# Kernel optimization log

Hardware: AMD Instinct MI355X
Metric: run time of the kernel (lower is better)

Reference implementation:

```python
import jax, jax.numpy as jnp
import numpy as np

N = 4096
D = 256
THRESH = 0.04  # default threshold arg of MultiLayerGCN.forward


def setup_inputs() -> dict:
    key = jax.random.key(0)
    ks = jax.random.split(key, 6)
    A = jax.random.normal(ks[0], (N, N), dtype=jnp.float32)
    features = jax.random.normal(ks[1], (N, D), dtype=jnp.float32)
    s = 0.02
    W1 = jax.random.normal(ks[2], (D, D), dtype=jnp.float32) * s
    b1 = jax.random.normal(ks[3], (D,), dtype=jnp.float32) * s
    W2 = jax.random.normal(ks[4], (D, D), dtype=jnp.float32) * s
    b2 = jax.random.normal(ks[5], (D,), dtype=jnp.float32) * s
    return {"A": A, "features": features, "W1": W1, "b1": b1, "W2": W2, "b2": b2}


def _graph_conv(C, out_isqrt, in_isqrt, h, W, b):
    # DGL GraphConv, norm='both': scale src by out_deg^-1/2, aggregate over
    # edges u->v (rst[v] = sum_u C[u,v] * h[u]), scale dst by in_deg^-1/2.
    h = (h * out_isqrt[:, None]) @ W            # [N, out]
    agg = jnp.einsum('uv,ud->vd', C, h)          # C^T @ h, honoring edge direction
    return agg * in_isqrt[:, None] + b


def reference(A, features, W1, b1, W2, b2):
    dt = features.dtype
    mask = (A >= THRESH).astype(dt)
    # add_edges(nodes, nodes) adds self loops on top of surviving diagonal -> counts
    C = mask + jnp.eye(A.shape[0], dtype=dt)
    out_deg = jnp.maximum(C.sum(axis=1), 1.0)    # clamp(min=1) as in DGL
    in_deg = jnp.maximum(C.sum(axis=0), 1.0)
    out_isqrt = jax.lax.rsqrt(out_deg)
    in_isqrt = jax.lax.rsqrt(in_deg)
    h1 = jax.nn.relu(_graph_conv(C, out_isqrt, in_isqrt, features, W1, b1))
    h2 = jax.nn.relu(_graph_conv(C, out_isqrt, in_isqrt, h1, W2, b2))
    return (h1, h2)
```

## Files before the change

kernel.cpp:

```cpp
#include <hip/hip_runtime.h>
#include <stdint.h>

#define NN 4096
#define DD 256
#define TH 0.04f

typedef __attribute__((ext_vector_type(4))) float f32x4;
typedef __attribute__((ext_vector_type(16))) float f32x16;
typedef __attribute__((ext_vector_type(8))) short s16x8;

__device__ __forceinline__ unsigned short f2bf(float f) {
  union { float f; uint32_t u; } x; x.f = f;
  uint32_t u = x.u;
  return (unsigned short)((u + 0x7FFFu + ((u >> 16) & 1u)) >> 16);
}
__device__ __forceinline__ float bf2f(unsigned short h) {
  union { uint32_t u; float f; } x; x.u = ((uint32_t)h) << 16;
  return x.f;
}

__global__ __launch_bounds__(256) void k_deg(const float* __restrict__ A,
                                             unsigned short* __restrict__ bitsT,
                                             unsigned char* __restrict__ colpart,
                                             float* __restrict__ oi,
                                             const float* __restrict__ W1,
                                             const float* __restrict__ W2,
                                             unsigned short* __restrict__ WTbP,
                                             unsigned short* __restrict__ W2TbP) {
  __shared__ unsigned short lds16[256 * 8];
  const int t = threadIdx.x, b = blockIdx.x;
  const int u0 = b * 8;
  uint32_t cs[16];
#pragma unroll
  for (int k = 0; k < 16; ++k) cs[k] = 0;
#pragma unroll
  for (int rb = 0; rb < 2; ++rb) {
    f32x4 a[4][4];
#pragma unroll
    for (int r = 0; r < 4; ++r) {
      const f32x4* p = reinterpret_cast<const f32x4*>(A + (size_t)(u0 + rb * 4 + r) * NN + t * 16);
#pragma unroll
      for (int c = 0; c < 4; ++c) a[r][c] = p[c];
    }
#pragma unroll
    for (int r = 0; r < 4; ++r) {
      uint32_t m = 0;
#pragma unroll
      for (int c = 0; c < 4; ++c)
#pragma unroll
        for (int j = 0; j < 4; ++j) m |= (a[r][c][j] >= TH ? 1u : 0u) << (c * 4 + j);
      lds16[t * 8 + rb * 4 + r] = (unsigned short)m;
#pragma unroll
      for (int k = 0; k < 16; ++k) cs[k] += (m >> k) & 1u;
    }
  }
  uint4 pk;
  pk.x = cs[0]  | (cs[1]  << 8) | (cs[2]  << 16) | (cs[3]  << 24);
  pk.y = cs[4]  | (cs[5]  << 8) | (cs[6]  << 16) | (cs[7]  << 24);
  pk.z = cs[8]  | (cs[9]  << 8) | (cs[10] << 16) | (cs[11] << 24);
  pk.w = cs[12] | (cs[13] << 8) | (cs[14] << 16) | (cs[15] << 24);
  *reinterpret_cast<uint4*>(colpart + (size_t)b * 4096 + t * 16) = pk;
  __syncthreads();
  uint4 wv4 = *reinterpret_cast<const uint4*>(&lds16[t * 8]);
  *reinterpret_cast<uint4*>(bitsT + (size_t)t * 4096 + u0) = wv4;
  if (t < 64) {
    const int r = t >> 3, part = t & 7;
    uint32_t s = 0;
#pragma unroll
    for (int wv = part * 32; wv < part * 32 + 32; ++wv)
      s += (uint32_t)__popc((uint32_t)lds16[wv * 8 + r]);
    s += __shfl_down(s, 4, 8);
    s += __shfl_down(s, 2, 8);
    s += __shfl_down(s, 1, 8);
    if (part == 0) oi[u0 + r] = rsqrtf((float)(s + 1u));
  }
  if (b < 32) {
    const float* W = (b < 16) ? W1 : W2;
    unsigned short* Wo = (b < 16) ? WTbP : W2TbP;
    const int base = (b & 15) * 4096 + t * 16;
#pragma unroll
    for (int e = 0; e < 16; ++e) {
      const int idx = base + e;
      const int frag = idx >> 9, pos = idx & 511;
      const int lc = pos >> 3, j = pos & 7;
      const int dt = frag >> 3, ks = frag & 7;
      const int k = ks * 32 + (lc >> 4) * 8 + j;
      const int d = dt * 16 + (lc & 15);
      Wo[idx] = f2bf(W[k * 256 + d]);
    }
  }
}

__global__ __launch_bounds__(256) void k_hw(const float* __restrict__ H,
                                            const float* __restrict__ oi,
                                            const unsigned short* __restrict__ WTbP,
                                            unsigned short* __restrict__ hWb,
                                            unsigned short* __restrict__ hWbP,
                                            const unsigned char* __restrict__ colpart,
                                            float* __restrict__ ii,
                                            int doii) {
  __shared__ unsigned short hs[16 * 264];
  __shared__ unsigned short lt[16 * 260];
  const int t = threadIdx.x;
  const int u0 = blockIdx.x * 16;
  if (doii) {
    const int v0 = blockIdx.x * 16;
    const int vI = t >> 4, g = t & 15;
    uint32_t s = 0;
#pragma unroll 8
    for (int r = g * 32; r < g * 32 + 32; ++r)
      s += colpart[(size_t)r * 4096 + v0 + vI];
    s += __shfl_down(s, 8, 16);
    s += __shfl_down(s, 4, 16);
    s += __shfl_down(s, 2, 16);
    s += __shfl_down(s, 1, 16);
    if (g == 0) ii[v0 + vI] = rsqrtf((float)(s + 1u));
  }
#pragma unroll
  for (int rep = 0; rep < 4; ++rep) {
    const int flat = rep * 256 + t;
    const int row = flat >> 6, c4 = flat & 63;
    f32x4 v = *reinterpret_cast<const f32x4*>(H + (size_t)(u0 + row) * DD + c4 * 4);
    const float sc = oi[u0 + row];
    uint2 pw;
    pw.x = (uint32_t)f2bf(v[0] * sc) | ((uint32_t)f2bf(v[1] * sc) << 16);
    pw.y = (uint32_t)f2bf(v[2] * sc) | ((uint32_t)f2bf(v[3] * sc) << 16);
    *reinterpret_cast<uint2*>(&hs[row * 264 + c4 * 4]) = pw;
  }
  __syncthreads();

  const int lane = t & 63, w = t >> 6, l15 = lane & 15, l4 = lane >> 4;
  const f32x4 z = {0.f, 0.f, 0.f, 0.f};
  f32x4 acc[4];
#pragma unroll
  for (int jn = 0; jn < 4; ++jn) acc[jn] = z;

#pragma unroll
  for (int ks = 0; ks < 8; ++ks) {
    s16x8 af = *reinterpret_cast<const s16x8*>(&hs[l15 * 264 + ks * 32 + l4 * 8]);
#pragma unroll
    for (int jn = 0; jn < 4; ++jn) {
      const int dt = w * 4 + jn;
      s16x8 bf = *reinterpret_cast<const s16x8*>(WTbP + ((size_t)dt * 8 + ks) * 512 + lane * 8);
      acc[jn] = __builtin_amdgcn_mfma_f32_16x16x32_bf16(af, bf, acc[jn], 0, 0, 0);
    }
  }
#pragma unroll
  for (int jn = 0; jn < 4; ++jn) {
    const int d = w * 64 + jn * 16 + l15;
#pragma unroll
    for (int r = 0; r < 4; ++r) {
      const int ul = l4 * 4 + r;
      unsigned short hv = f2bf(acc[jn][r]);
      hWb[(size_t)(u0 + ul) * DD + d] = hv;
      lt[ul * 260 + d] = hv;
    }
  }
  __syncthreads();
  const int sg = u0 >> 4;
#pragma unroll
  for (int cc = 0; cc < 2; ++cc) {
    const int c = t * 2 + cc;
    const int dt = c >> 6, lc = c & 63;
    const int ub = (lc >> 5) * 8;
    const int d = dt * 32 + (lc & 31);
    uint4 val;
    val.x = (uint32_t)lt[(ub + 0) * 260 + d] | ((uint32_t)lt[(ub + 1) * 260 + d] << 16);
    val.y = (uint32_t)lt[(ub + 2) * 260 + d] | ((uint32_t)lt[(ub + 3) * 260 + d] << 16);
    val.z = (uint32_t)lt[(ub + 4) * 260 + d] | ((uint32_t)lt[(ub + 5) * 260 + d] << 16);
    val.w = (uint32_t)lt[(ub + 6) * 260 + d] | ((uint32_t)lt[(ub + 7) * 260 + d] << 16);
    *reinterpret_cast<uint4*>(hWbP + ((size_t)dt * 256 + sg) * 512 + lc * 8) = val;
  }
}

__global__ __launch_bounds__(512, 2) void k_spmm(const unsigned short* __restrict__ bitsT,
                                                 const unsigned short* __restrict__ hWbP,
                                                 const unsigned short* __restrict__ hWb,
                                                 const float* __restrict__ ii,
                                                 const float* __restrict__ bias,
                                                 float* __restrict__ dst) {
  __shared__ float lds[4 * 64 * 68];
  const int t = threadIdx.x, bb = blockIdx.x;
  const int lane = t & 63, w = t >> 6;
  const int mi = w & 1, kc = w >> 1;
  const int xcd = bb & 7, jj = bb >> 3;
  const int vt = xcd * 8 + (jj >> 2), dq = jj & 3;
  const int V0 = vt * 64, D0 = dq * 64;
  const int l31 = lane & 31, l5 = lane >> 5;
  const uint32_t sh = lane & 15;
  const int wvl = vt * 4 + mi * 2 + ((lane >> 4) & 1);
  const unsigned short* Ab = bitsT + (size_t)wvl * 4096 + l5 * 8 + kc * 1024;
  const unsigned short* Bp0 = hWbP + ((size_t)(dq * 2 + 0) * 256 + kc * 64) * 512 + lane * 8;
  const unsigned short* Bp1 = hWbP + ((size_t)(dq * 2 + 1) * 256 + kc * 64) * 512 + lane * 8;

  f32x16 acc0, acc1;
#pragma unroll
  for (int q = 0; q < 16; ++q) { acc0[q] = 0.f; acc1[q] = 0.f; }

  uint4 h0 = *reinterpret_cast<const uint4*>(Ab);
  s16x8 p00 = *reinterpret_cast<const s16x8*>(Bp0);
  s16x8 p10 = *reinterpret_cast<const s16x8*>(Bp1);
  uint4 h1 = *reinterpret_cast<const uint4*>(Ab + 16);
  s16x8 p01 = *reinterpret_cast<const s16x8*>(Bp0 + 512);
  s16x8 p11 = *reinterpret_cast<const s16x8*>(Bp1 + 512);

#pragma unroll 1
  for (int it = 0; it < 32; ++it) {
    union { s16x8 v; uint32_t u[4]; } af0;
    af0.u[0] = ((h0.x >> sh) & 0x10001u) * 0x3F80u;
    af0.u[1] = ((h0.y >> sh) & 0x10001u) * 0x3F80u;
    af0.u[2] = ((h0.z >> sh) & 0x10001u) * 0x3F80u;
    af0.u[3] = ((h0.w >> sh) & 0x10001u) * 0x3F80u;
    acc0 = __builtin_amdgcn_mfma_f32_32x32x16_bf16(af0.v, p00, acc0, 0, 0, 0);
    acc1 = __builtin_amdgcn_mfma_f32_32x32x16_bf16(af0.v, p10, acc1, 0, 0, 0);
    const int s0 = (it * 2 + 2) & 63;
    h0 = *reinterpret_cast<const uint4*>(Ab + s0 * 16);
    p00 = *reinterpret_cast<const s16x8*>(Bp0 + s0 * 512);
    p10 = *reinterpret_cast<const s16x8*>(Bp1 + s0 * 512);
    union { s16x8 v; uint32_t u[4]; } af1;
    af1.u[0] = ((h1.x >> sh) & 0x10001u) * 0x3F80u;
    af1.u[1] = ((h1.y >> sh) & 0x10001u) * 0x3F80u;
    af1.u[2] = ((h1.z >> sh) & 0x10001u) * 0x3F80u;
    af1.u[3] = ((h1.w >> sh) & 0x10001u) * 0x3F80u;
    acc0 = __builtin_amdgcn_mfma_f32_32x32x16_bf16(af1.v, p01, acc0, 0, 0, 0);
    acc1 = __builtin_amdgcn_mfma_f32_32x32x16_bf16(af1.v, p11, acc1, 0, 0, 0);
    const int s1 = (it * 2 + 3) & 63;
    h1 = *reinterpret_cast<const uint4*>(Ab + s1 * 16);
    p01 = *reinterpret_cast<const s16x8*>(Bp0 + s1 * 512);
    p11 = *reinterpret_cast<const s16x8*>(Bp1 + s1 * 512);
  }

  float* buf = lds + (size_t)kc * (64 * 68);
#pragma unroll
  for (int reg = 0; reg < 16; ++reg) {
    const int row = (reg & 3) + 8 * (reg >> 2) + 4 * l5;
    buf[(mi * 32 + row) * 68 + l31] = acc0[reg];
    buf[(mi * 32 + row) * 68 + 32 + l31] = acc1[reg];
  }
  __syncthreads();

  const int vloc = t >> 3, d8 = (t & 7) * 8;
  const int v = V0 + vloc;
  const float* base = lds + vloc * 68 + d8;
  f32x4 s0v = *reinterpret_cast<const f32x4*>(base);
  f32x4 s1v = *reinterpret_cast<const f32x4*>(base + 4);
#pragma unroll
  for (int q = 1; q < 4; ++q) {
    s0v += *reinterpret_cast<const f32x4*>(base + q * (64 * 68));
    s1v += *reinterpret_cast<const f32x4*>(base + q * (64 * 68) + 4);
  }
  union { s16x8 v; unsigned short us[8]; } self;
  self.v = *reinterpret_cast<const s16x8*>(hWb + (size_t)v * DD + D0 + d8);
  const float iv = ii[v];
  const f32x4 bi0 = *reinterpret_cast<const f32x4*>(bias + D0 + d8);
  const f32x4 bi1 = *reinterpret_cast<const f32x4*>(bias + D0 + d8 + 4);
  f32x4 o0, o1;
#pragma unroll
  for (int e = 0; e < 4; ++e) {
    o0[e] = fmaxf((s0v[e] + bf2f(self.us[e])) * iv + bi0[e], 0.f);
    o1[e] = fmaxf((s1v[e] + bf2f(self.us[e + 4])) * iv + bi1[e], 0.f);
  }
  f32x4* po = reinterpret_cast<f32x4*>(dst + (size_t)v * DD + D0 + d8);
  po[0] = o0; po[1] = o1;
}

extern "C" void kernel_launch(void* const* d_in, const int* in_sizes, int n_in,
                              void* d_out, int out_size, void* d_ws, size_t ws_size,
                              hipStream_t stream) {
  const float* A    = (const float*)d_in[0];
  const float* feat = (const float*)d_in[1];
  const float* W1   = (const float*)d_in[2];
  const float* b1   = (const float*)d_in[3];
  const float* W2   = (const float*)d_in[4];
  const float* b2   = (const float*)d_in[5];
  float* out = (float*)d_out;
  char* ws = (char*)d_ws;

  unsigned short* bitsT   = (unsigned short*)ws;
  unsigned char*  colpart = (unsigned char*)(ws + (2u << 20));
  unsigned short* hWbP    = (unsigned short*)(ws + (4u << 20));
  unsigned short* hWb     = (unsigned short*)(ws + (6u << 20));
  unsigned short* WTbP    = (unsigned short*)(ws + (8u << 20));
  unsigned short* W2TbP   = (unsigned short*)(ws + (8u << 20) + (1u << 17));
  float*          oi      = (float*)(ws + (8u << 20) + (2u << 17));
  float*          ii      = oi + NN;

  k_deg<<<512, 256, 0, stream>>>(A, bitsT, colpart, oi, W1, W2, WTbP, W2TbP);

  k_hw<<<256, 256, 0, stream>>>(feat, oi, WTbP, hWb, hWbP, colpart, ii, 1);
  k_spmm<<<256, 512, 0, stream>>>(bitsT, hWbP, hWb, ii, b1, out);

  k_hw<<<256, 256, 0, stream>>>(out, oi, W2TbP, hWb, hWbP, colpart, ii, 0);
  k_spmm<<<256, 512, 0, stream>>>(bitsT, hWbP, hWb, ii, b2, out + (size_t)NN * DD);
}
```

Baseline: 75.00 us.

## Fuse first feature transform into scan kernel and move src-degree scaling into SpMM

Merges the threshold-scan kernel with the first H·W1 transform by giving extra blocks to the transform, which removes one launch and lets both stages overlap. The out-degree scaling is no longer applied to H before the GEMM. Instead a bf16 copy of out_isqrt is multiplied into the expanded adjacency bits inside the SpMM, and the self-loop term is scaled in the epilogue. In-degree computation moves from k_hw into the first SpMM. W is now converted and transposed through LDS per k-step inside each transform block rather than prepacked once, which adds redundant conversion work and extra syncs per block, and rounding out_isqrt to bf16 costs some accuracy.

```diff
diff --git a/kernel.cpp b/kernel.cpp
--- a/kernel.cpp
+++ b/kernel.cpp
@@ -8,26 +8,108 @@
 typedef __attribute__((ext_vector_type(4))) float f32x4;
 typedef __attribute__((ext_vector_type(16))) float f32x16;
 typedef __attribute__((ext_vector_type(8))) short s16x8;
-
-__device__ __forceinline__ unsigned short f2bf(float f) {
+typedef unsigned short us;
+
+__device__ __forceinline__ us f2bf(float f) {
   union { float f; uint32_t u; } x; x.f = f;
   uint32_t u = x.u;
-  return (unsigned short)((u + 0x7FFFu + ((u >> 16) & 1u)) >> 16);
-}
-__device__ __forceinline__ float bf2f(unsigned short h) {
+  return (us)((u + 0x7FFFu + ((u >> 16) & 1u)) >> 16);
+}
+__device__ __forceinline__ float bf2f(us h) {
   union { uint32_t u; float f; } x; x.u = ((uint32_t)h) << 16;
   return x.f;
 }
 
-__global__ __launch_bounds__(256) void k_deg(const float* __restrict__ A,
-                                             unsigned short* __restrict__ bitsT,
-                                             unsigned char* __restrict__ colpart,
-                                             float* __restrict__ oi,
-                                             const float* __restrict__ W1,
-                                             const float* __restrict__ W2,
-                                             unsigned short* __restrict__ WTbP,
-                                             unsigned short* __restrict__ W2TbP) {
-  __shared__ unsigned short lds16[256 * 8];
+__device__ __forceinline__ void hw_block(const float* __restrict__ H,
+                                         const float* __restrict__ W,
+                                         int u0,
+                                         us* __restrict__ hWb,
+                                         us* __restrict__ hWbP,
+                                         char* smem) {
+  us (*hs)[264] = reinterpret_cast<us(*)[264]>(smem);
+  us (*wt)[34]  = reinterpret_cast<us(*)[34]>(smem + 16 * 264 * 2);
+  us (*lt)[260] = reinterpret_cast<us(*)[260]>(smem + 16 * 264 * 2 + 256 * 34 * 2);
+  const int t = threadIdx.x;
+#pragma unroll
+  for (int rep = 0; rep < 4; ++rep) {
+    const int flat = rep * 256 + t;
+    const int row = flat >> 6, c4 = (flat & 63) * 4;
+    f32x4 v = *reinterpret_cast<const f32x4*>(H + (size_t)(u0 + row) * DD + c4);
+    uint2 pw;
+    pw.x = (uint32_t)f2bf(v[0]) | ((uint32_t)f2bf(v[1]) << 16);
+    pw.y = (uint32_t)f2bf(v[2]) | ((uint32_t)f2bf(v[3]) << 16);
+    *reinterpret_cast<uint2*>(&hs[row][c4]) = pw;
+  }
+  const int lane = t & 63, w = t >> 6, l15 = lane & 15, l4 = lane >> 4;
+  const f32x4 z = {0.f, 0.f, 0.f, 0.f};
+  f32x4 acc[4];
+#pragma unroll
+  for (int jn = 0; jn < 4; ++jn) acc[jn] = z;
+#pragma unroll 1
+  for (int ks = 0; ks < 8; ++ks) {
+    __syncthreads();
+#pragma unroll
+    for (int rr = 0; rr < 8; ++rr) {
+      const int flat = rr * 256 + t;
+      const int k = flat >> 6, d0 = (flat & 63) * 4;
+      f32x4 wv = *reinterpret_cast<const f32x4*>(W + (size_t)(ks * 32 + k) * DD + d0);
+      wt[d0 + 0][k] = f2bf(wv[0]);
+      wt[d0 + 1][k] = f2bf(wv[1]);
+      wt[d0 + 2][k] = f2bf(wv[2]);
+      wt[d0 + 3][k] = f2bf(wv[3]);
+    }
+    __syncthreads();
+    s16x8 af = *reinterpret_cast<const s16x8*>(&hs[l15][ks * 32 + l4 * 8]);
+#pragma unroll
+    for (int jn = 0; jn < 4; ++jn) {
+      const int dt = w * 4 + jn;
+      s16x8 bf = *reinterpret_cast<const s16x8*>(&wt[dt * 16 + l15][l4 * 8]);
+      acc[jn] = __builtin_amdgcn_mfma_f32_16x16x32_bf16(af, bf, acc[jn], 0, 0, 0);
+    }
+  }
+#pragma unroll
+  for (int jn = 0; jn < 4; ++jn) {
+    const int d = w * 64 + jn * 16 + l15;
+#pragma unroll
+    for (int r = 0; r < 4; ++r) {
+      const int ul = l4 * 4 + r;
+      us hv = f2bf(acc[jn][r]);
+      hWb[(size_t)(u0 + ul) * DD + d] = hv;
+      lt[ul][d] = hv;
+    }
+  }
+  __syncthreads();
+  const int sg = u0 >> 4;
+#pragma unroll
+  for (int cc = 0; cc < 2; ++cc) {
+    const int c = t * 2 + cc;
+    const int dt = c >> 6, lc = c & 63;
+    const int ub = (lc >> 5) * 8;
+    const int d = dt * 32 + (lc & 31);
+    uint4 val;
+    val.x = (uint32_t)lt[ub + 0][d] | ((uint32_t)lt[ub + 1][d] << 16);
+    val.y = (uint32_t)lt[ub + 2][d] | ((uint32_t)lt[ub + 3][d] << 16);
+    val.z = (uint32_t)lt[ub + 4][d] | ((uint32_t)lt[ub + 5][d] << 16);
+    val.w = (uint32_t)lt[ub + 6][d] | ((uint32_t)lt[ub + 7][d] << 16);
+    *reinterpret_cast<uint4*>(hWbP + ((size_t)dt * 256 + sg) * 512 + lc * 8) = val;
+  }
+}
+
+__global__ __launch_bounds__(256) void k_scanhw1(const float* __restrict__ A,
+                                                 const float* __restrict__ feat,
+                                                 const float* __restrict__ W1,
+                                                 us* __restrict__ bitsT,
+                                                 unsigned char* __restrict__ colpart,
+                                                 float* __restrict__ oif,
+                                                 us* __restrict__ oib,
+                                                 us* __restrict__ hWb,
+                                                 us* __restrict__ hWbP) {
+  __shared__ __align__(16) char smem[34176];
+  if (blockIdx.x >= 512) {
+    hw_block(feat, W1, (blockIdx.x - 512) * 16, hWb, hWbP, smem);
+    return;
+  }
+  us* lds16 = reinterpret_cast<us*>(smem);
   const int t = threadIdx.x, b = blockIdx.x;
   const int u0 = b * 8;
   uint32_t cs[16];
@@ -49,7 +131,7 @@
       for (int c = 0; c < 4; ++c)
 #pragma unroll
         for (int j = 0; j < 4; ++j) m |= (a[r][c][j] >= TH ? 1u : 0u) << (c * 4 + j);
-      lds16[t * 8 + rb * 4 + r] = (unsigned short)m;
+      lds16[t * 8 + rb * 4 + r] = (us)m;
 #pragma unroll
       for (int k = 0; k < 16; ++k) cs[k] += (m >> k) & 1u;
     }
@@ -72,170 +154,138 @@
     s += __shfl_down(s, 4, 8);
     s += __shfl_down(s, 2, 8);
     s += __shfl_down(s, 1, 8);
-    if (part == 0) oi[u0 + r] = rsqrtf((float)(s + 1u));
-  }
-  if (b < 32) {
-    const float* W = (b < 16) ? W1 : W2;
-    unsigned short* Wo = (b < 16) ? WTbP : W2TbP;
-    const int base = (b & 15) * 4096 + t * 16;
-#pragma unroll
-    for (int e = 0; e < 16; ++e) {
-      const int idx = base + e;
-      const int frag = idx >> 9, pos = idx & 511;
-      const int lc = pos >> 3, j = pos & 7;
-      const int dt = frag >> 3, ks = frag & 7;
-      const int k = ks * 32 + (lc >> 4) * 8 + j;
-      const int d = dt * 16 + (lc & 15);
-      Wo[idx] = f2bf(W[k * 256 + d]);
+    if (part == 0) {
+      float val = rsqrtf((float)(s + 1u));
+      oif[u0 + r] = val;
+      oib[u0 + r] = f2bf(val);
     }
   }
 }
 
 __global__ __launch_bounds__(256) void k_hw(const float* __restrict__ H,
-                                            const float* __restrict__ oi,
-                                            const unsigned short* __restrict__ WTbP,
-                                            unsigned short* __restrict__ hWb,
-                                            unsigned short* __restrict__ hWbP,
-                                            const unsigned char* __restrict__ colpart,
-                                            float* __restrict__ ii,
-                                            int doii) {
-  __shared__ unsigned short hs[16 * 264];
-  __shared__ unsigned short lt[16 * 260];
-  const int t = threadIdx.x;
-  const int u0 = blockIdx.x * 16;
-  if (doii) {
-    const int v0 = blockIdx.x * 16;
-    const int vI = t >> 4, g = t & 15;
-    uint32_t s = 0;
-#pragma unroll 8
-    for (int r = g * 32; r < g * 32 + 32; ++r)
-      s += colpart[(size_t)r * 4096 + v0 + vI];
-    s += __shfl_down(s, 8, 16);
-    s += __shfl_down(s, 4, 16);
-    s += __shfl_down(s, 2, 16);
-    s += __shfl_down(s, 1, 16);
-    if (g == 0) ii[v0 + vI] = rsqrtf((float)(s + 1u));
-  }
-#pragma unroll
-  for (int rep = 0; rep < 4; ++rep) {
-    const int flat = rep * 256 + t;
-    const int row = flat >> 6, c4 = flat & 63;
-    f32x4 v = *reinterpret_cast<const f32x4*>(H + (size_t)(u0 + row) * DD + c4 * 4);
-    const float sc = oi[u0 + row];
-    uint2 pw;
-    pw.x = (uint32_t)f2bf(v[0] * sc) | ((uint32_t)f2bf(v[1] * sc) << 16);
-    pw.y = (uint32_t)f2bf(v[2] * sc) | ((uint32_t)f2bf(v[3] * sc) << 16);
-    *reinterpret_cast<uint2*>(&hs[row * 264 + c4 * 4]) = pw;
-  }
-  __syncthreads();
-
-  const int lane = t & 63, w = t >> 6, l15 = lane & 15, l4 = lane >> 4;
-  const f32x4 z = {0.f, 0.f, 0.f, 0.f};
-  f32x4 acc[4];
-#pragma unroll
-  for (int jn = 0; jn < 4; ++jn) acc[jn] = z;
-
-#pragma unroll
-  for (int ks = 0; ks < 8; ++ks) {
-    s16x8 af = *reinterpret_cast<const s16x8*>(&hs[l15 * 264 + ks * 32 + l4 * 8]);
-#pragma unroll
-    for (int jn = 0; jn < 4; ++jn) {
-      const int dt = w * 4 + jn;
-      s16x8 bf = *reinterpret_cast<const s16x8*>(WTbP + ((size_t)dt * 8 + ks) * 512 + lane * 8);
-      acc[jn] = __builtin_amdgcn_mfma_f32_16x16x32_bf16(af, bf, acc[jn], 0, 0, 0);
-    }
-  }
-#pragma unroll
-  for (int jn = 0; jn < 4; ++jn) {
-    const int d = w * 64 + jn * 16 + l15;
-#pragma unroll
-    for (int r = 0; r < 4; ++r) {
-      const int ul = l4 * 4 + r;
-      unsigned short hv = f2bf(acc[jn][r]);
-      hWb[(size_t)(u0 + ul) * DD + d] = hv;
-      lt[ul * 260 + d] = hv;
-    }
-  }
-  __syncthreads();
-  const int sg = u0 >> 4;
-#pragma unroll
-  for (int cc = 0; cc < 2; ++cc) {
-    const int c = t * 2 + cc;
-    const int dt = c >> 6, lc = c & 63;
-    const int ub = (lc >> 5) * 8;
-    const int d = dt * 32 + (lc & 31);
-    uint4 val;
-    val.x = (uint32_t)lt[(ub + 0) * 260 + d] | ((uint32_t)lt[(ub + 1) * 260 + d] << 16);
-    val.y = (uint32_t)lt[(ub + 2) * 260 + d] | ((uint32_t)lt[(ub + 3) * 260 + d] << 16);
-    val.z = (uint32_t)lt[(ub + 4) * 260 + d] | ((uint32_t)lt[(ub + 5) * 260 + d] << 16);
-    val.w = (uint32_t)lt[(ub + 6) * 260 + d] | ((uint32_t)lt[(ub + 7) * 260 + d] << 16);
-    *reinterpret_cast<uint4*>(hWbP + ((size_t)dt * 256 + sg) * 512 + lc * 8) = val;
-  }
-}
-
-__global__ __launch_bounds__(512, 2) void k_spmm(const unsigned short* __restrict__ bitsT,
-                                                 const unsigned short* __restrict__ hWbP,
-                                                 const unsigned short* __restrict__ hWb,
-                                                 const float* __restrict__ ii,
+                                            const float* __restrict__ W,
+                                            us* __restrict__ hWb,
+                                            us* __restrict__ hWbP) {
+  __shared__ __align__(16) char smem[34176];
+  hw_block(H, W, blockIdx.x * 16, hWb, hWbP, smem);
+}
+
+__global__ __launch_bounds__(512, 2) void k_spmm(const us* __restrict__ bitsT,
+                                                 const us* __restrict__ hWbP,
+                                                 const us* __restrict__ hWb,
+                                                 const float* __restrict__ oif,
+                                                 const us* __restrict__ oib,
+                                                 const unsigned char* __restrict__ colpart,
+                                                 float* __restrict__ ii_g,
                                                  const float* __restrict__ bias,
-                                                 float* __restrict__ dst) {
+                                                 float* __restrict__ dst,
+                                                 int doii) {
   __shared__ float lds[4 * 64 * 68];
+  __shared__ float ii_s[64];
   const int t = threadIdx.x, bb = blockIdx.x;
   const int lane = t & 63, w = t >> 6;
-  const int mi = w & 1, kc = w >> 1;
+  const int kc = w >> 1, dn = w & 1;
   const int xcd = bb & 7, jj = bb >> 3;
   const int vt = xcd * 8 + (jj >> 2), dq = jj & 3;
   const int V0 = vt * 64, D0 = dq * 64;
+
+  if (doii) {
+    uint32_t* sc = reinterpret_cast<uint32_t*>(lds);
+    const int v4 = t & 15, c = t >> 4;
+    uint32_t s0 = 0, s1 = 0;
+#pragma unroll 4
+    for (int r = 0; r < 16; ++r) {
+      uint32_t x = *reinterpret_cast<const uint32_t*>(colpart + (size_t)(c * 16 + r) * 4096 + V0 + v4 * 4);
+      s0 += x & 0x00FF00FFu;
+      s1 += (x >> 8) & 0x00FF00FFu;
+    }
+    sc[(c * 16 + v4) * 2] = s0;
+    sc[(c * 16 + v4) * 2 + 1] = s1;
+    __syncthreads();
+    if (t < 64) {
+      const int v4b = t >> 2, sub = t & 3;
+      const int reg = sub & 1, hi = sub >> 1;
+      uint32_t s = 0;
+#pragma unroll
+      for (int cc = 0; cc < 32; ++cc)
+        s += (sc[(cc * 16 + v4b) * 2 + reg] >> (hi * 16)) & 0xFFFFu;
+      float val = rsqrtf((float)(s + 1u));
+      ii_s[t] = val;
+      ii_g[V0 + t] = val;
+    }
+    __syncthreads();
+  } else {
+    if (t < 64) ii_s[t] = ii_g[V0 + t];
+    __syncthreads();
+  }
+
   const int l31 = lane & 31, l5 = lane >> 5;
   const uint32_t sh = lane & 15;
-  const int wvl = vt * 4 + mi * 2 + ((lane >> 4) & 1);
-  const unsigned short* Ab = bitsT + (size_t)wvl * 4096 + l5 * 8 + kc * 1024;
-  const unsigned short* Bp0 = hWbP + ((size_t)(dq * 2 + 0) * 256 + kc * 64) * 512 + lane * 8;
-  const unsigned short* Bp1 = hWbP + ((size_t)(dq * 2 + 1) * 256 + kc * 64) * 512 + lane * 8;
+  const int wsel = (lane >> 4) & 1;
+  const us* A0 = bitsT + (size_t)(vt * 4 + wsel) * 4096 + kc * 1024 + l5 * 8;
+  const us* A1 = bitsT + (size_t)(vt * 4 + 2 + wsel) * 4096 + kc * 1024 + l5 * 8;
+  const us* Ob = oib + kc * 1024 + l5 * 8;
+  const int dt = dq * 2 + dn;
+  const us* Bp = hWbP + ((size_t)dt * 256 + kc * 64) * 512 + lane * 8;
 
   f32x16 acc0, acc1;
 #pragma unroll
   for (int q = 0; q < 16; ++q) { acc0[q] = 0.f; acc1[q] = 0.f; }
 
-  uint4 h0 = *reinterpret_cast<const uint4*>(Ab);
-  s16x8 p00 = *reinterpret_cast<const s16x8*>(Bp0);
-  s16x8 p10 = *reinterpret_cast<const s16x8*>(Bp1);
-  uint4 h1 = *reinterpret_cast<const uint4*>(Ab + 16);
-  s16x8 p01 = *reinterpret_cast<const s16x8*>(Bp0 + 512);
-  s16x8 p11 = *reinterpret_cast<const s16x8*>(Bp1 + 512);
+  uint4 h0a = *reinterpret_cast<const uint4*>(A0);
+  uint4 h1a = *reinterpret_cast<const uint4*>(A1);
+  s16x8 oa = *reinterpret_cast<const s16x8*>(Ob);
+  s16x8 pa = *reinterpret_cast<const s16x8*>(Bp);
+  uint4 h0b = *reinterpret_cast<const uint4*>(A0 + 16);
+  uint4 h1b = *reinterpret_cast<const uint4*>(A1 + 16);
+  s16x8 ob = *reinterpret_cast<const s16x8*>(Ob + 16);
+  s16x8 pb = *reinterpret_cast<const s16x8*>(Bp + 512);
+
+#define XPAND(AF, H, O)                                                        \
+  {                                                                            \
+    const uint32_t* ou = reinterpret_cast<const uint32_t*>(&(O));              \
+    uint32_t m_;                                                               \
+    m_ = (((H).x >> sh) & 0x10001u) * 0xFFFFu; AF.u[0] = ou[0] & m_;           \
+    m_ = (((H).y >> sh) & 0x10001u) * 0xFFFFu; AF.u[1] = ou[1] & m_;           \
+    m_ = (((H).z >> sh) & 0x10001u) * 0xFFFFu; AF.u[2] = ou[2] & m_;           \
+    m_ = (((H).w >> sh) & 0x10001u) * 0xFFFFu; AF.u[3] = ou[3] & m_;           \
+  }
 
 #pragma unroll 1
   for (int it = 0; it < 32; ++it) {
-    union { s16x8 v; uint32_t u[4]; } af0;
-    af0.u[0] = ((h0.x >> sh) & 0x10001u) * 0x3F80u;
-    af0.u[1] = ((h0.y >> sh) & 0x10001u) * 0x3F80u;
-    af0.u[2] = ((h0.z >> sh) & 0x10001u) * 0x3F80u;
-    af0.u[3] = ((h0.w >> sh) & 0x10001u) * 0x3F80u;
-    acc0 = __builtin_amdgcn_mfma_f32_32x32x16_bf16(af0.v, p00, acc0, 0, 0, 0);
-    acc1 = __builtin_amdgcn_mfma_f32_32x32x16_bf16(af0.v, p10, acc1, 0, 0, 0);
-    const int s0 = (it * 2 + 2) & 63;
-    h0 = *reinterpret_cast<const uint4*>(Ab + s0 * 16);
-    p00 = *reinterpret_cast<const s16x8*>(Bp0 + s0 * 512);
-    p10 = *reinterpret_cast<const s16x8*>(Bp1 + s0 * 512);
-    union { s16x8 v; uint32_t u[4]; } af1;
-    af1.u[0] = ((h1.x >> sh) & 0x10001u) * 0x3F80u;
-    af1.u[1] = ((h1.y >> sh) & 0x10001u) * 0x3F80u;
-    af1.u[2] = ((h1.z >> sh) & 0x10001u) * 0x3F80u;
-    af1.u[3] = ((h1.w >> sh) & 0x10001u) * 0x3F80u;
-    acc0 = __builtin_amdgcn_mfma_f32_32x32x16_bf16(af1.v, p01, acc0, 0, 0, 0);
-    acc1 = __builtin_amdgcn_mfma_f32_32x32x16_bf16(af1.v, p11, acc1, 0, 0, 0);
-    const int s1 = (it * 2 + 3) & 63;
-    h1 = *reinterpret_cast<const uint4*>(Ab + s1 * 16);
-    p01 = *reinterpret_cast<const s16x8*>(Bp0 + s1 * 512);
-    p11 = *reinterpret_cast<const s16x8*>(Bp1 + s1 * 512);
-  }
+    {
+      union { s16x8 v; uint32_t u[4]; } af0, af1;
+      XPAND(af0, h0a, oa);
+      XPAND(af1, h1a, oa);
+      acc0 = __builtin_amdgcn_mfma_f32_32x32x16_bf16(af0.v, pa, acc0, 0, 0, 0);
+      acc1 = __builtin_amdgcn_mfma_f32_32x32x16_bf16(af1.v, pa, acc1, 0, 0, 0);
+      const int sA = (it * 2 + 2) & 63;
+      h0a = *reinterpret_cast<const uint4*>(A0 + sA * 16);
+      h1a = *reinterpret_cast<const uint4*>(A1 + sA * 16);
+      oa = *reinterpret_cast<const s16x8*>(Ob + sA * 16);
+      pa = *reinterpret_cast<const s16x8*>(Bp + (size_t)sA * 512);
+    }
+    {
+      union { s16x8 v; uint32_t u[4]; } af0, af1;
+      XPAND(af0, h0b, ob);
+      XPAND(af1, h1b, ob);
+      acc0 = __builtin_amdgcn_mfma_f32_32x32x16_bf16(af0.v, pb, acc0, 0, 0, 0);
+      acc1 = __builtin_amdgcn_mfma_f32_32x32x16_bf16(af1.v, pb, acc1, 0, 0, 0);
+      const int sB = (it * 2 + 3) & 63;
+      h0b = *reinterpret_cast<const uint4*>(A0 + sB * 16);
+      h1b = *reinterpret_cast<const uint4*>(A1 + sB * 16);
+      ob = *reinterpret_cast<const s16x8*>(Ob + sB * 16);
+      pb = *reinterpret_cast<const s16x8*>(Bp + (size_t)sB * 512);
+    }
+  }
+#undef XPAND
 
   float* buf = lds + (size_t)kc * (64 * 68);
 #pragma unroll
   for (int reg = 0; reg < 16; ++reg) {
     const int row = (reg & 3) + 8 * (reg >> 2) + 4 * l5;
-    buf[(mi * 32 + row) * 68 + l31] = acc0[reg];
-    buf[(mi * 32 + row) * 68 + 32 + l31] = acc1[reg];
+    buf[row * 68 + dn * 32 + l31] = acc0[reg];
+    buf[(32 + row) * 68 + dn * 32 + l31] = acc1[reg];
   }
   __syncthreads();
 
@@ -249,16 +299,17 @@
     s0v += *reinterpret_cast<const f32x4*>(base + q * (64 * 68));
     s1v += *reinterpret_cast<const f32x4*>(base + q * (64 * 68) + 4);
   }
-  union { s16x8 v; unsigned short us[8]; } self;
+  union { s16x8 v; us u[8]; } self;
   self.v = *reinterpret_cast<const s16x8*>(hWb + (size_t)v * DD + D0 + d8);
-  const float iv = ii[v];
+  const float iv = ii_s[vloc];
+  const float ov = oif[v];
   const f32x4 bi0 = *reinterpret_cast<const f32x4*>(bias + D0 + d8);
   const f32x4 bi1 = *reinterpret_cast<const f32x4*>(bias + D0 + d8 + 4);
   f32x4 o0, o1;
 #pragma unroll
   for (int e = 0; e < 4; ++e) {
-    o0[e] = fmaxf((s0v[e] + bf2f(self.us[e])) * iv + bi0[e], 0.f);
-    o1[e] = fmaxf((s1v[e] + bf2f(self.us[e + 4])) * iv + bi1[e], 0.f);
+    o0[e] = fmaxf((s0v[e] + ov * bf2f(self.u[e])) * iv + bi0[e], 0.f);
+    o1[e] = fmaxf((s1v[e] + ov * bf2f(self.u[e + 4])) * iv + bi1[e], 0.f);
   }
   f32x4* po = reinterpret_cast<f32x4*>(dst + (size_t)v * DD + D0 + d8);
   po[0] = o0; po[1] = o1;
@@ -276,20 +327,17 @@
   float* out = (float*)d_out;
   char* ws = (char*)d_ws;
 
-  unsigned short* bitsT   = (unsigned short*)ws;
-  unsigned char*  colpart = (unsigned char*)(ws + (2u << 20));
-  unsigned short* hWbP    = (unsigned short*)(ws + (4u << 20));
-  unsigned short* hWb     = (unsigned short*)(ws + (6u << 20));
-  unsigned short* WTbP    = (unsigned short*)(ws + (8u << 20));
-  unsigned short* W2TbP   = (unsigned short*)(ws + (8u << 20) + (1u << 17));
-  float*          oi      = (float*)(ws + (8u << 20) + (2u << 17));
-  float*          ii      = oi + NN;
-
-  k_deg<<<512, 256, 0, stream>>>(A, bitsT, colpart, oi, W1, W2, WTbP, W2TbP);
-
-  k_hw<<<256, 256, 0, stream>>>(feat, oi, WTbP, hWb, hWbP, colpart, ii, 1);
-  k_spmm<<<256, 512, 0, stream>>>(bitsT, hWbP, hWb, ii, b1, out);
-
-  k_hw<<<256, 256, 0, stream>>>(out, oi, W2TbP, hWb, hWbP, colpart, ii, 0);
-  k_spmm<<<256, 512, 0, stream>>>(bitsT, hWbP, hWb, ii, b2, out + (size_t)NN * DD);
-}
+  us*            bitsT   = (us*)ws;
+  unsigned char* colpart = (unsigned char*)(ws + (2u << 20));
+  us*            hWbP    = (us*)(ws + (4u << 20));
+  us*            hWb     = (us*)(ws + (6u << 20));
+  float*         oif     = (float*)(ws + (8u << 20));
+  us*            oib     = (us*)(ws + (8u << 20) + (16u << 10));
+  float*         ii_g    = (float*)(ws + (8u << 20) + (24u << 10));
+
+  k_scanhw1<<<768, 256, 0, stream>>>(A, feat, W1, bitsT, colpart, oif, oib, hWb, hWbP);
+  k_spmm<<<256, 512, 0, stream>>>(bitsT, hWbP, hWb, oif, oib, colpart, ii_g, b1, out, 1);
+  k_hw<<<256, 256, 0, stream>>>(out, W2, hWb, hWbP);
+  k_spmm<<<256, 512, 0, stream>>>(bitsT, hWbP, hWb, oif, oib, colpart, ii_g, b2,
+                                  out + (size_t)NN * DD, 0);
+}
```

Result: slower. 86.33 us (+15.1%).
